# Optimization experiments

Hardware: AMD Instinct MI355X
Metric: run time of the kernel (lower is better)

## Reference

```python
import jax, jax.numpy as jnp
import numpy as np

N = 50000   # nodes
E = 800000  # directed edges
D = 128     # input_feat_dim
H = 128     # hidden1
L = 3       # GatedGraphConv layers
G = 64      # num graphs in batch
NEG_SLOPE = 0.01


def setup_inputs() -> dict:
    key = jax.random.key(0)
    ks = jax.random.split(key, 12)
    s = 1.0 / np.sqrt(H)
    x = jax.random.normal(ks[0], (N, D), jnp.float32)
    edge_index = jax.random.randint(ks[1], (2, E), 0, N)
    batch = jnp.sort(jax.random.randint(ks[2], (N,), 0, G))
    W_gcn = jax.random.normal(ks[3], (D, H), jnp.float32) * s
    b_gcn = jnp.zeros((H,), jnp.float32)
    W_gg = jax.random.normal(ks[4], (L, H, H), jnp.float32) * s   # GatedGraphConv per-layer weight
    W_ih = jax.random.normal(ks[5], (3 * H, H), jnp.float32) * s  # GRUCell input weights (r,z,n)
    W_hh = jax.random.normal(ks[6], (3 * H, H), jnp.float32) * s  # GRUCell hidden weights
    b_ih = jnp.zeros((3 * H,), jnp.float32)
    b_hh = jnp.zeros((3 * H,), jnp.float32)
    W1 = jax.random.normal(ks[7], (H, H), jnp.float32) * s
    b1 = jnp.zeros((H,), jnp.float32)
    W2 = jax.random.normal(ks[8], (H, 1), jnp.float32) * s
    b2 = jnp.zeros((1,), jnp.float32)
    return dict(x=x, edge_index=edge_index, batch=batch, W_gcn=W_gcn, b_gcn=b_gcn,
                W_gg=W_gg, W_ih=W_ih, W_hh=W_hh, b_ih=b_ih, b_hh=b_hh,
                W1=W1, b1=b1, W2=W2, b2=b2)


def _seg(vals, idx, num):
    return jax.ops.segment_sum(vals, idx, num_segments=num)


def _gcn(x, row, col, W, b):
    # PyG GCNConv: add self loops, symmetric norm, aggregate at target (col)
    xw = x @ W
    deg = _seg(jnp.ones((E,), xw.dtype), col, N) + 1.0  # +1 for self loop
    dinv = jax.lax.rsqrt(deg)
    norm = dinv[row] * dinv[col]                         # [E]
    out = _seg(xw[row] * norm[:, None], col, N)          # gather-scale-scatter
    out = out + xw * (dinv * dinv)[:, None]              # self-loop term
    return out + b


def _gru(m, h, W_ih, W_hh, b_ih, b_hh):
    gi = m @ W_ih.T + b_ih
    gh = h @ W_hh.T + b_hh
    ir, iz, inn = jnp.split(gi, 3, axis=-1)
    hr, hz, hn = jnp.split(gh, 3, axis=-1)
    r = jax.nn.sigmoid(ir + hr)
    z = jax.nn.sigmoid(iz + hz)
    n = jnp.tanh(inn + r * hn)
    return (1.0 - z) * n + z * h


def reference(x, edge_index, batch, W_gcn, b_gcn, W_gg, W_ih, W_hh, b_ih, b_hh, W1, b1, W2, b2):
    row, col = edge_index[0], edge_index[1]
    h = jax.nn.leaky_relu(_gcn(x, row, col, W_gcn, b_gcn), NEG_SLOPE)   # [N,H]
    g = h
    for l in range(L):  # GatedGraphConv: message = x_j @ W_l, sum-aggregate at col, GRU update
        m = _seg((g @ W_gg[l])[row], col, N)
        g = _gru(m, g, W_ih, W_hh, b_ih, b_hh)
    h = jax.nn.leaky_relu(g, NEG_SLOPE) + h
    h = jax.nn.leaky_relu(h @ W1 + b1, NEG_SLOPE)
    probs = jax.nn.sigmoid(h @ W2 + b2)                                  # [N,1]
    # maxcut loss: per-graph expected cut
    degrees = _seg(jnp.ones((E,), probs.dtype), row, N)[:, None]         # degree(row) per node
    expected_weight = _seg(probs[row] * probs[col], batch[row], G)       # [G,1]
    expected_degree = _seg(probs * degrees, batch, G)                    # [G,1]
    return -(expected_degree - expected_weight) / 2.0                    # [G,1]
```

## Files before the change

kernel.cpp:

```cpp
#include <hip/hip_runtime.h>
#include <math.h>

#define HD 128
#define NEG 0.01f
#define GD 64
#define LDST 136

typedef short bf16x8 __attribute__((ext_vector_type(8)));
typedef float floatx4 __attribute__((ext_vector_type(4)));

__device__ __forceinline__ unsigned short f2bf(float f) {
    unsigned int u = __float_as_uint(f);
    u += 0x7fffu + ((u >> 16) & 1u);
    return (unsigned short)(u >> 16);
}
__device__ __forceinline__ float bf2f(unsigned short b) {
    return __uint_as_float(((unsigned int)b) << 16);
}
__device__ __forceinline__ float sigm(float v) { return 1.f / (1.f + __expf(-v)); }

__device__ __forceinline__ void mm64(const unsigned short* __restrict__ ap,
                                     const unsigned short* __restrict__ W,
                                     int m16, int quad, floatx4* acc) {
    #pragma unroll
    for (int ks = 0; ks < 4; ks++) {
        const int koff = ks * 32 + quad * 8;
        bf16x8 a = *(const bf16x8*)(ap + koff);
        #pragma unroll
        for (int cg = 0; cg < 8; cg++) {
            bf16x8 b = *(const bf16x8*)(W + (size_t)(cg * 16 + m16) * HD + koff);
            acc[cg] = __builtin_amdgcn_mfma_f32_16x16x32_bf16(a, b, acc[cg], 0, 0, 0);
        }
    }
}

__device__ __forceinline__ void loadB(const unsigned short* __restrict__ W,
                                      int w, int m16, int quad, bf16x8 bf[2][4]) {
    #pragma unroll
    for (int cgl = 0; cgl < 2; cgl++)
        #pragma unroll
        for (int ks = 0; ks < 4; ks++)
            bf[cgl][ks] = *(const bf16x8*)(W + (size_t)((2 * w + cgl) * 16 + m16) * HD
                                           + ks * 32 + quad * 8);
}
__device__ __forceinline__ void mmAcc(const unsigned short* __restrict__ Atile,
                                      int m16, int quad, const bf16x8 bf[2][4],
                                      floatx4 acc[4][2]) {
    #pragma unroll
    for (int rg = 0; rg < 4; rg++)
        #pragma unroll
        for (int ks = 0; ks < 4; ks++) {
            bf16x8 a = *(const bf16x8*)(Atile + (rg * 16 + m16) * LDST + ks * 32 + quad * 8);
            acc[rg][0] = __builtin_amdgcn_mfma_f32_16x16x32_bf16(a, bf[0][ks], acc[rg][0], 0, 0, 0);
            acc[rg][1] = __builtin_amdgcn_mfma_f32_16x16x32_bf16(a, bf[1][ks], acc[rg][1], 0, 0, 0);
        }
}

__global__ __launch_bounds__(256) void gemm_mfma(
    const unsigned short* __restrict__ A, const unsigned short* __restrict__ BT,
    float* __restrict__ C32, unsigned short* __restrict__ C16, int M)
{
    __shared__ unsigned short As[128 * LDST];
    __shared__ unsigned short Bs[128 * LDST];
    const int tid = threadIdx.x;
    const int r0 = blockIdx.x * 128;
    {
        int rowi = tid >> 1, half = tid & 1;
        int gr = r0 + rowi; if (gr >= M) gr = M - 1;
        const float4* sa = (const float4*)(A + (size_t)gr * HD + half * 64);
        float4* da = (float4*)(As + rowi * LDST + half * 64);
        const float4* sb = (const float4*)(BT + (size_t)rowi * HD + half * 64);
        float4* db = (float4*)(Bs + rowi * LDST + half * 64);
        #pragma unroll
        for (int i = 0; i < 8; i++) { da[i] = sa[i]; db[i] = sb[i]; }
    }
    __syncthreads();
    const int wave = tid >> 6, lane = tid & 63;
    const int m16 = lane & 15, quad = lane >> 4;
    floatx4 acc[2][8];
    #pragma unroll
    for (int i = 0; i < 2; i++)
        #pragma unroll
        for (int j = 0; j < 8; j++) acc[i][j] = (floatx4){0.f, 0.f, 0.f, 0.f};
    const unsigned short* ar0 = As + (wave * 32 + m16) * LDST;
    const unsigned short* ar1 = As + (wave * 32 + 16 + m16) * LDST;
    #pragma unroll
    for (int ks = 0; ks < 4; ks++) {
        const int koff = ks * 32 + quad * 8;
        bf16x8 a0 = *(const bf16x8*)(ar0 + koff);
        bf16x8 a1 = *(const bf16x8*)(ar1 + koff);
        #pragma unroll
        for (int cg = 0; cg < 8; cg++) {
            bf16x8 b = *(const bf16x8*)(Bs + (cg * 16 + m16) * LDST + koff);
            acc[0][cg] = __builtin_amdgcn_mfma_f32_16x16x32_bf16(a0, b, acc[0][cg], 0, 0, 0);
            acc[1][cg] = __builtin_amdgcn_mfma_f32_16x16x32_bf16(a1, b, acc[1][cg], 0, 0, 0);
        }
    }
    #pragma unroll
    for (int rg = 0; rg < 2; rg++)
        #pragma unroll
        for (int cg = 0; cg < 8; cg++)
            #pragma unroll
            for (int i = 0; i < 4; i++) {
                int r = r0 + wave * 32 + rg * 16 + quad * 4 + i;
                if (r >= M) continue;
                int c = cg * 16 + m16;
                float v = acc[rg][cg][i];
                if (C32) C32[(size_t)r * HD + c] = v;
                C16[(size_t)r * HD + c] = f2bf(v);
            }
}

__global__ __launch_bounds__(256) void k_gather_gcn(
    const unsigned short* __restrict__ src, const float* __restrict__ xw,
    const int* __restrict__ csr, const int* __restrict__ offs,
    const float* __restrict__ dinv, const float* __restrict__ bias,
    float* __restrict__ h, unsigned short* __restrict__ g16, int N)
{
    int node = blockIdx.x * 4 + (threadIdx.x >> 6);
    if (node >= N) return;
    int lane = threadIdx.x & 63;
    int s = offs[node], e = offs[node + 1];
    float ax = 0.f, ay = 0.f;
    int j = s;
    for (; j + 4 <= e; j += 4) {
        int r0 = csr[j], r1 = csr[j + 1], r2 = csr[j + 2], r3 = csr[j + 3];
        unsigned int u0 = *(const unsigned int*)(src + (size_t)r0 * HD + lane * 2);
        unsigned int u1 = *(const unsigned int*)(src + (size_t)r1 * HD + lane * 2);
        unsigned int u2 = *(const unsigned int*)(src + (size_t)r2 * HD + lane * 2);
        unsigned int u3 = *(const unsigned int*)(src + (size_t)r3 * HD + lane * 2);
        float s0 = dinv[r0], s1 = dinv[r1], s2 = dinv[r2], s3 = dinv[r3];
        ax += __uint_as_float(u0 << 16) * s0 + __uint_as_float(u1 << 16) * s1
            + __uint_as_float(u2 << 16) * s2 + __uint_as_float(u3 << 16) * s3;
        ay += __uint_as_float(u0 & 0xffff0000u) * s0 + __uint_as_float(u1 & 0xffff0000u) * s1
            + __uint_as_float(u2 & 0xffff0000u) * s2 + __uint_as_float(u3 & 0xffff0000u) * s3;
    }
    for (; j < e; j++) {
        int r = csr[j];
        unsigned int u = *(const unsigned int*)(src + (size_t)r * HD + lane * 2);
        float sc = dinv[r];
        ax += __uint_as_float(u << 16) * sc;
        ay += __uint_as_float(u & 0xffff0000u) * sc;
    }
    float dn = dinv[node];
    float dv2 = dn * dn;
    size_t i = (size_t)node * HD + lane * 2;
    float v0 = ax * dn + xw[i] * dv2 + bias[lane * 2];
    float v1 = ay * dn + xw[i + 1] * dv2 + bias[lane * 2 + 1];
    v0 = v0 > 0.f ? v0 : v0 * NEG;
    v1 = v1 > 0.f ? v1 : v1 * NEG;
    h[i] = v0; h[i + 1] = v1;
    *(unsigned int*)(g16 + i) = (unsigned int)f2bf(v0) | ((unsigned int)f2bf(v1) << 16);
}

__global__ __launch_bounds__(256) void k_gather_m(
    const unsigned short* __restrict__ src, const int* __restrict__ csr,
    const int* __restrict__ offs, unsigned short* __restrict__ out16, int N)
{
    int node = blockIdx.x * 4 + (threadIdx.x >> 6);
    if (node >= N) return;
    int lane = threadIdx.x & 63;
    int s = offs[node], e = offs[node + 1];
    float ax = 0.f, ay = 0.f;
    int j = s;
    for (; j + 4 <= e; j += 4) {
        int r0 = csr[j], r1 = csr[j + 1], r2 = csr[j + 2], r3 = csr[j + 3];
        unsigned int u0 = *(const unsigned int*)(src + (size_t)r0 * HD + lane * 2);
        unsigned int u1 = *(const unsigned int*)(src + (size_t)r1 * HD + lane * 2);
        unsigned int u2 = *(const unsigned int*)(src + (size_t)r2 * HD + lane * 2);
        unsigned int u3 = *(const unsigned int*)(src + (size_t)r3 * HD + lane * 2);
        ax += __uint_as_float(u0 << 16) + __uint_as_float(u1 << 16)
            + __uint_as_float(u2 << 16) + __uint_as_float(u3 << 16);
        ay += __uint_as_float(u0 & 0xffff0000u) + __uint_as_float(u1 & 0xffff0000u)
            + __uint_as_float(u2 & 0xffff0000u) + __uint_as_float(u3 & 0xffff0000u);
    }
    for (; j < e; j++) {
        int r = csr[j];
        unsigned int u = *(const unsigned int*)(src + (size_t)r * HD + lane * 2);
        ax += __uint_as_float(u << 16);
        ay += __uint_as_float(u & 0xffff0000u);
    }
    unsigned int p = (unsigned int)f2bf(ax) | ((unsigned int)f2bf(ay) << 16);
    *(unsigned int*)(out16 + (size_t)node * HD + lane * 2) = p;
}

__global__ __launch_bounds__(256, 4) void k_gru_gates(
    const unsigned short* __restrict__ m_bf, const unsigned short* __restrict__ g_bf,
    const unsigned short* __restrict__ Wih, const unsigned short* __restrict__ Whh,
    const float* __restrict__ b_ih, const float* __restrict__ b_hh,
    const float* __restrict__ g_in, float* __restrict__ g_out,
    unsigned short* __restrict__ g16_out, int M)
{
    __shared__ unsigned short Am[64 * LDST];
    __shared__ unsigned short Ag[64 * LDST];
    const int tid = threadIdx.x;
    const int r0 = blockIdx.x * 64;
    {
        int rowi = tid >> 2, q = tid & 3;
        int gr = r0 + rowi; if (gr >= M) gr = M - 1;
        const float4* sm = (const float4*)(m_bf + (size_t)gr * HD + q * 32);
        const float4* sg = (const float4*)(g_bf + (size_t)gr * HD + q * 32);
        float4* dm = (float4*)(Am + rowi * LDST + q * 32);
        float4* dg = (float4*)(Ag + rowi * LDST + q * 32);
        #pragma unroll
        for (int i = 0; i < 4; i++) { dm[i] = sm[i]; dg[i] = sg[i]; }
    }
    __syncthreads();
    const int w = tid >> 6, l = tid & 63;
    const int m16 = l & 15, quad = l >> 4;

    floatx4 accA[4][2], accB[4][2];
    bf16x8 bf[2][4];
    #pragma unroll
    for (int rg = 0; rg < 4; rg++)
        #pragma unroll
        for (int c = 0; c < 2; c++) {
            accA[rg][c] = (floatx4){0.f, 0.f, 0.f, 0.f};
            accB[rg][c] = (floatx4){0.f, 0.f, 0.f, 0.f};
        }
    loadB(Wih, w, m16, quad, bf);
    mmAcc(Am, m16, quad, bf, accA);
    loadB(Whh, w, m16, quad, bf);
    mmAcc(Ag, m16, quad, bf, accA);
    loadB(Whh + 256 * HD, w, m16, quad, bf);
    mmAcc(Ag, m16, quad, bf, accB);
    #pragma unroll
    for (int cgl = 0; cgl < 2; cgl++) {
        int c = (2 * w + cgl) * 16 + m16;
        float br = b_ih[c] + b_hh[c];
        float bhn = b_hh[256 + c];
        #pragma unroll
        for (int rg = 0; rg < 4; rg++)
            #pragma unroll
            for (int i = 0; i < 4; i++) {
                float r = sigm(accA[rg][cgl][i] + br);
                accB[rg][cgl][i] = r * (accB[rg][cgl][i] + bhn);
            }
    }
    loadB(Wih + 256 * HD, w, m16, quad, bf);
    mmAcc(Am, m16, quad, bf, accB);
    #pragma unroll
    for (int rg = 0; rg < 4; rg++)
        #pragma unroll
        for (int c = 0; c < 2; c++) accA[rg][c] = (floatx4){0.f, 0.f, 0.f, 0.f};
    loadB(Wih + 128 * HD, w, m16, quad, bf);
    mmAcc(Am, m16, quad, bf, accA);
    loadB(Whh + 128 * HD, w, m16, quad, bf);
    mmAcc(Ag, m16, quad, bf, accA);
    #pragma unroll
    for (int cgl = 0; cgl < 2; cgl++) {
        int c = (2 * w + cgl) * 16 + m16;
        float bz = b_ih[128 + c] + b_hh[128 + c];
        float bin = b_ih[256 + c];
        #pragma unroll
        for (int rg = 0; rg < 4; rg++)
            #pragma unroll
            for (int i = 0; i < 4; i++) {
                int r = r0 + rg * 16 + quad * 4 + i;
                if (r >= M) continue;
                float z = sigm(accA[rg][cgl][i] + bz);
                float n = tanhf(accB[rg][cgl][i] + bin);
                float gv = g_in[(size_t)r * HD + c];
                float o = (1.f - z) * n + z * gv;
                g_out[(size_t)r * HD + c] = o;
                g16_out[(size_t)r * HD + c] = f2bf(o);
            }
    }
}

__global__ __launch_bounds__(256, 4) void k_head_fused(
    const float* __restrict__ g, const float* __restrict__ h,
    const unsigned short* __restrict__ W1T, const float* __restrict__ b1,
    const float* __restrict__ W2, const float* __restrict__ b2,
    float* __restrict__ probs, int M)
{
    __shared__ unsigned short As[64 * LDST];
    const int tid = threadIdx.x;
    const int r0 = blockIdx.x * 64;
    {
        int rowi = tid >> 2, q = tid & 3;
        int gr = r0 + rowi; if (gr >= M) gr = M - 1;
        const float* gp = g + (size_t)gr * HD + q * 32;
        const float* hp = h + (size_t)gr * HD + q * 32;
        unsigned short* dst = As + rowi * LDST + q * 32;
        #pragma unroll
        for (int i = 0; i < 32; i += 4) {
            float4 gv = *(const float4*)(gp + i);
            float4 hv = *(const float4*)(hp + i);
            ushort4 o;
            float v;
            v = gv.x > 0.f ? gv.x : gv.x * NEG; o.x = f2bf(v + hv.x);
            v = gv.y > 0.f ? gv.y : gv.y * NEG; o.y = f2bf(v + hv.y);
            v = gv.z > 0.f ? gv.z : gv.z * NEG; o.z = f2bf(v + hv.z);
            v = gv.w > 0.f ? gv.w : gv.w * NEG; o.w = f2bf(v + hv.w);
            *(ushort4*)(dst + i) = o;
        }
    }
    __syncthreads();
    const int w = tid >> 6, l = tid & 63;
    const int m16 = l & 15, quad = l >> 4;
    floatx4 acc[8];
    #pragma unroll
    for (int j = 0; j < 8; j++) acc[j] = (floatx4){0.f, 0.f, 0.f, 0.f};
    mm64(As + (w * 16 + m16) * LDST, W1T, m16, quad, acc);
    #pragma unroll
    for (int i = 0; i < 4; i++) {
        float s = 0.f;
        #pragma unroll
        for (int cg = 0; cg < 8; cg++) {
            int c = cg * 16 + m16;
            float v = acc[cg][i] + b1[c];
            v = v > 0.f ? v : v * NEG;
            s += v * W2[c];
        }
        s += __shfl_xor(s, 1); s += __shfl_xor(s, 2);
        s += __shfl_xor(s, 4); s += __shfl_xor(s, 8);
        int r = r0 + w * 16 + quad * 4 + i;
        if (m16 == 0 && r < M) probs[r] = sigm(s + b2[0]);
    }
}

__global__ void k_prep_w(const float* __restrict__ W_gcn, const float* __restrict__ W_gg,
                         const float* __restrict__ W_ih, const float* __restrict__ W_hh,
                         const float* __restrict__ W1, unsigned short* __restrict__ Wq) {
    int i = blockIdx.x * blockDim.x + threadIdx.x;
    if (i >= 180224) return;
    float v;
    if (i < 16384) {
        int n = i >> 7, k = i & 127;
        v = W_gcn[k * 128 + n];
    } else if (i < 65536) {
        int j = i - 16384;
        int l = j >> 14, rr = j & 16383;
        int n = rr >> 7, k = rr & 127;
        v = W_gg[l * 16384 + k * 128 + n];
    } else if (i < 114688) {
        v = W_ih[i - 65536];
    } else if (i < 163840) {
        v = W_hh[i - 114688];
    } else {
        int j = i - 163840;
        int n = j >> 7, k = j & 127;
        v = W1[k * 128 + n];
    }
    Wq[i] = f2bf(v);
}

__global__ void k_cast_x(const float* __restrict__ s, unsigned short* __restrict__ d, int n2) {
    int i = blockIdx.x * blockDim.x + threadIdx.x;
    if (i >= n2) return;
    float2 v = *(const float2*)(s + (size_t)i * 2);
    unsigned int p = (unsigned int)f2bf(v.x) | ((unsigned int)f2bf(v.y) << 16);
    *(unsigned int*)(d + (size_t)i * 2) = p;
}

__global__ void k_hist(const int* __restrict__ col, int* __restrict__ cnt4,
                       int* __restrict__ rank, int N, int E) {
    int e = blockIdx.x * blockDim.x + threadIdx.x;
    if (e < E) {
        int s = blockIdx.x & 3;
        rank[e] = atomicAdd(&cnt4[s * N + col[e]], 1);
    }
}

#define SCHUNK 2048
__global__ __launch_bounds__(256) void k_scan1(const int* __restrict__ cnt4,
                                               int* __restrict__ excl,
                                               int* __restrict__ bsum, int N) {
    __shared__ int ts[256];
    int t = threadIdx.x;
    int base = blockIdx.x * SCHUNK + t * 8;
    int v[8]; int s = 0;
    #pragma unroll
    for (int q = 0; q < 8; q++) {
        int i = base + q;
        v[q] = (i < N) ? (cnt4[i] + cnt4[N + i] + cnt4[2 * N + i] + cnt4[3 * N + i]) : 0;
        s += v[q];
    }
    ts[t] = s;
    __syncthreads();
    for (int off = 1; off < 256; off <<= 1) {
        int a = (t >= off) ? ts[t - off] : 0;
        __syncthreads();
        ts[t] += a;
        __syncthreads();
    }
    int run = ts[t] - s;
    #pragma unroll
    for (int q = 0; q < 8; q++) { int i = base + q; if (i < N) excl[i] = run; run += v[q]; }
    if (t == 255) bsum[blockIdx.x] = ts[255];
}

__global__ void k_scan2(int* bsum, int nb) {
    if (threadIdx.x == 0) {
        int run = 0;
        for (int b = 0; b < nb; b++) { int v = bsum[b]; bsum[b] = run; run += v; }
    }
}

__global__ void k_csrfin(const int* __restrict__ excl, const int* __restrict__ bsum,
                         const int* __restrict__ cnt4, int* __restrict__ offs,
                         int* __restrict__ sbase, float* __restrict__ dinv, int N, int E) {
    int i = blockIdx.x * blockDim.x + threadIdx.x;
    if (i >= N) return;
    int o = excl[i] + bsum[i >> 11];
    offs[i] = o;
    if (i == 0) offs[N] = E;
    int c0 = cnt4[i], c1 = cnt4[N + i], c2 = cnt4[2 * N + i], c3 = cnt4[3 * N + i];
    sbase[i] = o;
    sbase[N + i] = o + c0;
    sbase[2 * N + i] = o + c0 + c1;
    sbase[3 * N + i] = o + c0 + c1 + c2;
    dinv[i] = rsqrtf((float)(c0 + c1 + c2 + c3) + 1.f);
}

__global__ void k_fill(const int* __restrict__ row, const int* __restrict__ col,
                       const int* __restrict__ sbase, const int* __restrict__ rank,
                       int* __restrict__ csr_rows, int N, int E) {
    int e = blockIdx.x * blockDim.x + threadIdx.x;
    if (e >= E) return;
    int s = (e >> 8) & 3;
    csr_rows[sbase[s * N + col[e]] + rank[e]] = row[e];
}

__global__ __launch_bounds__(256) void k_loss_edge(const float* __restrict__ probs,
                                                   const int* __restrict__ row,
                                                   const int* __restrict__ col,
                                                   const int* __restrict__ batch,
                                                   float* __restrict__ ed,
                                                   float* __restrict__ ew, int E) {
    __shared__ float bd[GD], be[GD];
    if (threadIdx.x < GD) { bd[threadIdx.x] = 0.f; be[threadIdx.x] = 0.f; }
    __syncthreads();
    for (int e = blockIdx.x * blockDim.x + threadIdx.x; e < E; e += gridDim.x * blockDim.x) {
        int r = row[e];
        float pr = probs[r];
        int b = batch[r];
        atomicAdd(&bd[b], pr);
        atomicAdd(&be[b], pr * probs[col[e]]);
    }
    __syncthreads();
    if (threadIdx.x < GD) {
        atomicAdd(&ed[threadIdx.x], bd[threadIdx.x]);
        atomicAdd(&ew[threadIdx.x], be[threadIdx.x]);
    }
}

__global__ void k_finalize(const float* __restrict__ ed, const float* __restrict__ ew,
                           float* __restrict__ out) {
    int g = threadIdx.x;
    if (g < GD) out[g] = -(ed[g] - ew[g]) * 0.5f;
}

extern "C" void kernel_launch(void* const* d_in, const int* in_sizes, int n_in,
                              void* d_out, int out_size, void* d_ws, size_t ws_size,
                              hipStream_t stream) {
    const float* x     = (const float*)d_in[0];
    const int*   ei    = (const int*)d_in[1];
    const int*   batch = (const int*)d_in[2];
    const float* W_gcn = (const float*)d_in[3];
    const float* b_gcn = (const float*)d_in[4];
    const float* W_gg  = (const float*)d_in[5];
    const float* W_ih  = (const float*)d_in[6];
    const float* W_hh  = (const float*)d_in[7];
    const float* b_ih  = (const float*)d_in[8];
    const float* b_hh  = (const float*)d_in[9];
    const float* W1    = (const float*)d_in[10];
    const float* b1    = (const float*)d_in[11];
    const float* W2    = (const float*)d_in[12];
    const float* b2    = (const float*)d_in[13];
    float* out = (float*)d_out;

    const int N = in_sizes[2];
    const int E = in_sizes[1] / 2;
    const int* row = ei;
    const int* col = ei + E;
    const size_t NH = (size_t)N * HD;

    float* F = (float*)d_ws;
    float* f_h  = F + 0 * NH;
    float* f_g  = F + 1 * NH;
    float* f_xw = F + 2 * NH;
    unsigned short* U = (unsigned short*)(F + 3 * NH);
    unsigned short* x_bf  = U;
    unsigned short* g_bf  = U + 1 * NH;
    unsigned short* t_bf  = U + 2 * NH;
    unsigned short* m_bf  = U + 3 * NH;
    unsigned short* Wq    = U + 4 * NH;
    unsigned short* WgcnT = Wq;
    unsigned short* WggT  = Wq + 16384;
    unsigned short* Wih16 = Wq + 65536;
    unsigned short* Whh16 = Wq + 114688;
    unsigned short* W1T   = Wq + 163840;
    float* S = (float*)(Wq + 180224);
    float* f_dinv  = S;
    float* f_probs = S + N;
    float* f_ed    = S + 2 * N;
    float* f_ew    = f_ed + GD;
    int* I = (int*)(f_ew + GD);
    int* i_cnt4  = I;
    int* i_excl  = I + 4 * N;
    int* i_offs  = I + 5 * N;
    int* i_bsum  = I + 6 * N + 8;
    int* i_sbase = I + 6 * N + 128;
    int* i_rank  = I + 10 * N + 128;
    int* i_csr   = i_rank + E;

    const int nb_scan = (N + SCHUNK - 1) / SCHUNK;
    const int gb64 = (N + 63) / 64;
    const int gb128 = (N + 127) / 128;
    const int eg = (E + 255) / 256;
    const int ng = (N + 255) / 256;
    const int gather_grid = (N + 3) / 4;

    hipMemsetAsync(i_cnt4, 0, sizeof(int) * 4 * (size_t)N, stream);
    hipMemsetAsync(f_ed, 0, sizeof(float) * 2 * GD, stream);

    k_prep_w<<<704, 256, 0, stream>>>(W_gcn, W_gg, W_ih, W_hh, W1, Wq);
    k_cast_x<<<(int)((NH / 2 + 255) / 256), 256, 0, stream>>>(x, x_bf, (int)(NH / 2));

    k_hist<<<eg, 256, 0, stream>>>(col, i_cnt4, i_rank, N, E);
    k_scan1<<<nb_scan, 256, 0, stream>>>(i_cnt4, i_excl, i_bsum, N);
    k_scan2<<<1, 64, 0, stream>>>(i_bsum, nb_scan);
    k_csrfin<<<ng, 256, 0, stream>>>(i_excl, i_bsum, i_cnt4, i_offs, i_sbase, f_dinv, N, E);
    k_fill<<<eg, 256, 0, stream>>>(row, col, i_sbase, i_rank, i_csr, N, E);

    gemm_mfma<<<gb128, 256, 0, stream>>>(x_bf, WgcnT, f_xw, t_bf, N);
    k_gather_gcn<<<gather_grid, 256, 0, stream>>>(t_bf, f_xw, i_csr, i_offs, f_dinv,
                                                  b_gcn, f_h, g_bf, N);

    for (int l = 0; l < 3; l++) {
        gemm_mfma<<<gb128, 256, 0, stream>>>(g_bf, WggT + (size_t)l * 16384,
                                             nullptr, t_bf, N);
        k_gather_m<<<gather_grid, 256, 0, stream>>>(t_bf, i_csr, i_offs, m_bf, N);
        k_gru_gates<<<gb64, 256, 0, stream>>>(m_bf, g_bf, Wih16, Whh16, b_ih, b_hh,
                                              (l == 0) ? f_h : f_g, f_g, g_bf, N);
    }

    k_head_fused<<<gb64, 256, 0, stream>>>(f_g, f_h, W1T, b1, W2, b2, f_probs, N);

    k_loss_edge<<<1024, 256, 0, stream>>>(f_probs, row, col, batch, f_ed, f_ew, E);
    k_finalize<<<1, 64, 0, stream>>>(f_ed, f_ew, out);
}
```

Before: 676.6 us.

## Drop fp32 GRU state, keep hidden in bf16 and stage coalesced GRU output

The GRU kernel now reads the previous hidden state from the bf16 tile already in shared memory and no longer reads or writes a separate fp32 copy. Output is staged through shared memory so each row is written to global memory in coalesced bf16 vectors. The head kernel reads the bf16 state instead of fp32. The GRU tile shrinks to 32 rows with a higher occupancy hint. Together these cut global traffic, at the cost of carrying the recurrent state in reduced precision across layers and giving each wave fewer MFMAs per B-fragment load.

```diff
diff --git a/kernel.cpp b/kernel.cpp
--- a/kernel.cpp
+++ b/kernel.cpp
@@ -5,6 +5,7 @@
 #define NEG 0.01f
 #define GD 64
 #define LDST 136
+#define FST 132
 
 typedef short bf16x8 __attribute__((ext_vector_type(8)));
 typedef float floatx4 __attribute__((ext_vector_type(4)));
@@ -43,11 +44,11 @@
             bf[cgl][ks] = *(const bf16x8*)(W + (size_t)((2 * w + cgl) * 16 + m16) * HD
                                            + ks * 32 + quad * 8);
 }
-__device__ __forceinline__ void mmAcc(const unsigned short* __restrict__ Atile,
-                                      int m16, int quad, const bf16x8 bf[2][4],
-                                      floatx4 acc[4][2]) {
-    #pragma unroll
-    for (int rg = 0; rg < 4; rg++)
+__device__ __forceinline__ void mmAcc32(const unsigned short* __restrict__ Atile,
+                                        int m16, int quad, const bf16x8 bf[2][4],
+                                        floatx4 acc[2][2]) {
+    #pragma unroll
+    for (int rg = 0; rg < 2; rg++)
         #pragma unroll
         for (int ks = 0; ks < 4; ks++) {
             bf16x8 a = *(const bf16x8*)(Atile + (rg * 16 + m16) * LDST + ks * 32 + quad * 8);
@@ -184,53 +185,53 @@
     *(unsigned int*)(out16 + (size_t)node * HD + lane * 2) = p;
 }
 
-__global__ __launch_bounds__(256, 4) void k_gru_gates(
+__global__ __launch_bounds__(256, 5) void k_gru_gates(
     const unsigned short* __restrict__ m_bf, const unsigned short* __restrict__ g_bf,
     const unsigned short* __restrict__ Wih, const unsigned short* __restrict__ Whh,
     const float* __restrict__ b_ih, const float* __restrict__ b_hh,
-    const float* __restrict__ g_in, float* __restrict__ g_out,
     unsigned short* __restrict__ g16_out, int M)
 {
-    __shared__ unsigned short Am[64 * LDST];
-    __shared__ unsigned short Ag[64 * LDST];
+    __shared__ unsigned short sh[2 * 32 * LDST];
+    unsigned short* Am = sh;
+    unsigned short* Ag = sh + 32 * LDST;
     const int tid = threadIdx.x;
-    const int r0 = blockIdx.x * 64;
+    const int r0 = blockIdx.x * 32;
     {
-        int rowi = tid >> 2, q = tid & 3;
+        int rowi = tid >> 3, q = tid & 7;
         int gr = r0 + rowi; if (gr >= M) gr = M - 1;
-        const float4* sm = (const float4*)(m_bf + (size_t)gr * HD + q * 32);
-        const float4* sg = (const float4*)(g_bf + (size_t)gr * HD + q * 32);
-        float4* dm = (float4*)(Am + rowi * LDST + q * 32);
-        float4* dg = (float4*)(Ag + rowi * LDST + q * 32);
-        #pragma unroll
-        for (int i = 0; i < 4; i++) { dm[i] = sm[i]; dg[i] = sg[i]; }
+        const float4* sm = (const float4*)(m_bf + (size_t)gr * HD + q * 16);
+        const float4* sg = (const float4*)(g_bf + (size_t)gr * HD + q * 16);
+        float4* dm = (float4*)(Am + rowi * LDST + q * 16);
+        float4* dg = (float4*)(Ag + rowi * LDST + q * 16);
+        dm[0] = sm[0]; dm[1] = sm[1];
+        dg[0] = sg[0]; dg[1] = sg[1];
     }
     __syncthreads();
     const int w = tid >> 6, l = tid & 63;
     const int m16 = l & 15, quad = l >> 4;
 
-    floatx4 accA[4][2], accB[4][2];
+    floatx4 accA[2][2], accB[2][2];
     bf16x8 bf[2][4];
     #pragma unroll
-    for (int rg = 0; rg < 4; rg++)
+    for (int rg = 0; rg < 2; rg++)
         #pragma unroll
         for (int c = 0; c < 2; c++) {
             accA[rg][c] = (floatx4){0.f, 0.f, 0.f, 0.f};
             accB[rg][c] = (floatx4){0.f, 0.f, 0.f, 0.f};
         }
     loadB(Wih, w, m16, quad, bf);
-    mmAcc(Am, m16, quad, bf, accA);
+    mmAcc32(Am, m16, quad, bf, accA);
     loadB(Whh, w, m16, quad, bf);
-    mmAcc(Ag, m16, quad, bf, accA);
+    mmAcc32(Ag, m16, quad, bf, accA);
     loadB(Whh + 256 * HD, w, m16, quad, bf);
-    mmAcc(Ag, m16, quad, bf, accB);
+    mmAcc32(Ag, m16, quad, bf, accB);
     #pragma unroll
     for (int cgl = 0; cgl < 2; cgl++) {
         int c = (2 * w + cgl) * 16 + m16;
         float br = b_ih[c] + b_hh[c];
         float bhn = b_hh[256 + c];
         #pragma unroll
-        for (int rg = 0; rg < 4; rg++)
+        for (int rg = 0; rg < 2; rg++)
             #pragma unroll
             for (int i = 0; i < 4; i++) {
                 float r = sigm(accA[rg][cgl][i] + br);
@@ -238,38 +239,62 @@
             }
     }
     loadB(Wih + 256 * HD, w, m16, quad, bf);
-    mmAcc(Am, m16, quad, bf, accB);
-    #pragma unroll
-    for (int rg = 0; rg < 4; rg++)
+    mmAcc32(Am, m16, quad, bf, accB);
+    #pragma unroll
+    for (int rg = 0; rg < 2; rg++)
         #pragma unroll
         for (int c = 0; c < 2; c++) accA[rg][c] = (floatx4){0.f, 0.f, 0.f, 0.f};
     loadB(Wih + 128 * HD, w, m16, quad, bf);
-    mmAcc(Am, m16, quad, bf, accA);
+    mmAcc32(Am, m16, quad, bf, accA);
     loadB(Whh + 128 * HD, w, m16, quad, bf);
-    mmAcc(Ag, m16, quad, bf, accA);
+    mmAcc32(Ag, m16, quad, bf, accA);
+    float ov[2][2][4];
     #pragma unroll
     for (int cgl = 0; cgl < 2; cgl++) {
         int c = (2 * w + cgl) * 16 + m16;
         float bz = b_ih[128 + c] + b_hh[128 + c];
         float bin = b_ih[256 + c];
         #pragma unroll
-        for (int rg = 0; rg < 4; rg++)
+        for (int rg = 0; rg < 2; rg++)
             #pragma unroll
             for (int i = 0; i < 4; i++) {
-                int r = r0 + rg * 16 + quad * 4 + i;
-                if (r >= M) continue;
                 float z = sigm(accA[rg][cgl][i] + bz);
                 float n = tanhf(accB[rg][cgl][i] + bin);
-                float gv = g_in[(size_t)r * HD + c];
-                float o = (1.f - z) * n + z * gv;
-                g_out[(size_t)r * HD + c] = o;
-                g16_out[(size_t)r * HD + c] = f2bf(o);
+                float gv = bf2f(Ag[(rg * 16 + quad * 4 + i) * LDST + c]);
+                ov[cgl][rg][i] = (1.f - z) * n + z * gv;
             }
     }
+    __syncthreads();
+    float* shf = (float*)sh;
+    #pragma unroll
+    for (int cgl = 0; cgl < 2; cgl++) {
+        int c = (2 * w + cgl) * 16 + m16;
+        #pragma unroll
+        for (int rg = 0; rg < 2; rg++)
+            #pragma unroll
+            for (int i = 0; i < 4; i++)
+                shf[(rg * 16 + quad * 4 + i) * FST + c] = ov[cgl][rg][i];
+    }
+    __syncthreads();
+    {
+        int rowi = tid >> 3, c0 = (tid & 7) * 16;
+        int gr = r0 + rowi;
+        if (gr < M) {
+            const float* srcp = shf + rowi * FST + c0;
+            unsigned short* dH = g16_out + (size_t)gr * HD + c0;
+            #pragma unroll
+            for (int k = 0; k < 16; k += 4) {
+                float4 v = *(const float4*)(srcp + k);
+                ushort4 ob;
+                ob.x = f2bf(v.x); ob.y = f2bf(v.y); ob.z = f2bf(v.z); ob.w = f2bf(v.w);
+                *(ushort4*)(dH + k) = ob;
+            }
+        }
+    }
 }
 
 __global__ __launch_bounds__(256, 4) void k_head_fused(
-    const float* __restrict__ g, const float* __restrict__ h,
+    const unsigned short* __restrict__ g_bf, const float* __restrict__ h,
     const unsigned short* __restrict__ W1T, const float* __restrict__ b1,
     const float* __restrict__ W2, const float* __restrict__ b2,
     float* __restrict__ probs, int M)
@@ -280,19 +305,19 @@
     {
         int rowi = tid >> 2, q = tid & 3;
         int gr = r0 + rowi; if (gr >= M) gr = M - 1;
-        const float* gp = g + (size_t)gr * HD + q * 32;
+        const unsigned short* gp = g_bf + (size_t)gr * HD + q * 32;
         const float* hp = h + (size_t)gr * HD + q * 32;
         unsigned short* dst = As + rowi * LDST + q * 32;
         #pragma unroll
         for (int i = 0; i < 32; i += 4) {
-            float4 gv = *(const float4*)(gp + i);
+            ushort4 gu = *(const ushort4*)(gp + i);
             float4 hv = *(const float4*)(hp + i);
             ushort4 o;
             float v;
-            v = gv.x > 0.f ? gv.x : gv.x * NEG; o.x = f2bf(v + hv.x);
-            v = gv.y > 0.f ? gv.y : gv.y * NEG; o.y = f2bf(v + hv.y);
-            v = gv.z > 0.f ? gv.z : gv.z * NEG; o.z = f2bf(v + hv.z);
-            v = gv.w > 0.f ? gv.w : gv.w * NEG; o.w = f2bf(v + hv.w);
+            v = bf2f(gu.x); v = v > 0.f ? v : v * NEG; o.x = f2bf(v + hv.x);
+            v = bf2f(gu.y); v = v > 0.f ? v : v * NEG; o.y = f2bf(v + hv.y);
+            v = bf2f(gu.z); v = v > 0.f ? v : v * NEG; o.z = f2bf(v + hv.z);
+            v = bf2f(gu.w); v = v > 0.f ? v : v * NEG; o.w = f2bf(v + hv.w);
             *(ushort4*)(dst + i) = o;
         }
     }
@@ -479,9 +504,8 @@
 
     float* F = (float*)d_ws;
     float* f_h  = F + 0 * NH;
-    float* f_g  = F + 1 * NH;
-    float* f_xw = F + 2 * NH;
-    unsigned short* U = (unsigned short*)(F + 3 * NH);
+    float* f_xw = F + 1 * NH;
+    unsigned short* U = (unsigned short*)(F + 2 * NH);
     unsigned short* x_bf  = U;
     unsigned short* g_bf  = U + 1 * NH;
     unsigned short* t_bf  = U + 2 * NH;
@@ -507,6 +531,7 @@
     int* i_csr   = i_rank + E;
 
     const int nb_scan = (N + SCHUNK - 1) / SCHUNK;
+    const int gb32 = (N + 31) / 32;
     const int gb64 = (N + 63) / 64;
     const int gb128 = (N + 127) / 128;
     const int eg = (E + 255) / 256;
@@ -533,11 +558,11 @@
         gemm_mfma<<<gb128, 256, 0, stream>>>(g_bf, WggT + (size_t)l * 16384,
                                              nullptr, t_bf, N);
         k_gather_m<<<gather_grid, 256, 0, stream>>>(t_bf, i_csr, i_offs, m_bf, N);
-        k_gru_gates<<<gb64, 256, 0, stream>>>(m_bf, g_bf, Wih16, Whh16, b_ih, b_hh,
-                                              (l == 0) ? f_h : f_g, f_g, g_bf, N);
-    }
-
-    k_head_fused<<<gb64, 256, 0, stream>>>(f_g, f_h, W1T, b1, W2, b2, f_probs, N);
+        k_gru_gates<<<gb32, 256, 0, stream>>>(m_bf, g_bf, Wih16, Whh16, b_ih, b_hh,
+                                              g_bf, N);
+    }
+
+    k_head_fused<<<gb64, 256, 0, stream>>>(g_bf, f_h, W1T, b1, W2, b2, f_probs, N);
 
     k_loss_edge<<<1024, 256, 0, stream>>>(f_probs, row, col, batch, f_ed, f_ew, E);
     k_finalize<<<1, 64, 0, stream>>>(f_ed, f_ew, out);
```

After: 615.5 us. 1.1x faster.
